# Kernel optimization log

Hardware: AMD Instinct MI355X
Metric: run time of the kernel (lower is better)

Reference implementation:

```python
import jax, jax.numpy as jnp
import numpy as np

H = 25  # fixed state size per module source
N_STEPS = 10


def _lstm_cell(x, h, c, W_ih, W_hh, b_ih, b_hh):
    # PyTorch LSTMCell: gates ordered i, f, g, o
    gates = x @ W_ih.T + b_ih + h @ W_hh.T + b_hh  # [B, 4H]
    i, f, g, o = jnp.split(gates, 4, axis=-1)
    c_new = jax.nn.sigmoid(f) * c + jax.nn.sigmoid(i) * jnp.tanh(g)
    h_new = jax.nn.sigmoid(o) * jnp.tanh(c_new)
    return h_new, c_new


def setup_inputs() -> dict:
    key = jax.random.key(0)
    ks = jax.random.split(key, 11)
    B, A = 131072, 18

    def u(k, shape, fan_in, fan_out):
        bound = np.sqrt(6.0 / (fan_in + fan_out)).astype(np.float32)
        return jax.random.uniform(k, shape, jnp.float32, -bound, bound)

    state = jax.random.normal(ks[0], (B, H), jnp.float32)
    # LSTMCell weights [4H, H]; biases zeroed per module init
    W_ih_enc = u(ks[1], (4 * H, H), H, 4 * H)
    W_hh_enc = u(ks[2], (4 * H, H), H, 4 * H)
    b_ih_enc = jnp.zeros((4 * H,), jnp.float32)
    b_hh_enc = jnp.zeros((4 * H,), jnp.float32)
    W_ih_dec = u(ks[3], (4 * H, H), H, 4 * H)
    W_hh_dec = u(ks[4], (4 * H, H), H, 4 * H)
    b_ih_dec = jnp.zeros((4 * H,), jnp.float32)
    b_hh_dec = jnp.zeros((4 * H,), jnp.float32)
    # actor head: norm_col_init std=0.01, bias 0
    w = jax.random.normal(ks[5], (A, H), jnp.float32)
    W_act = w * (0.01 / jnp.sqrt((w ** 2).sum(1, keepdims=True)))
    b_act = jnp.zeros((A,), jnp.float32)
    return {
        "state_repr_input": state,
        "W_ih_enc": W_ih_enc, "W_hh_enc": W_hh_enc, "b_ih_enc": b_ih_enc, "b_hh_enc": b_hh_enc,
        "W_ih_dec": W_ih_dec, "W_hh_dec": W_hh_dec, "b_ih_dec": b_ih_dec, "b_hh_dec": b_hh_dec,
        "W_act": W_act, "b_act": b_act,
    }


def reference(state_repr_input, W_ih_enc, W_hh_enc, b_ih_enc, b_hh_enc,
              W_ih_dec, W_hh_dec, b_ih_dec, b_hh_dec, W_act, b_act):
    B = state_repr_input.shape[0]
    zeros = jnp.zeros_like(state_repr_input)

    # Encoder: input to each step is previous hx (first step: state)
    def enc_step(carry, _):
        inp, h, c = carry
        h, c = _lstm_cell(inp, h, c, W_ih_enc, W_hh_enc, b_ih_enc, b_hh_enc)
        return (h, h, c), h

    (_, _, _), enc_hs = jax.lax.scan(enc_step, (state_repr_input, zeros, zeros), None, length=N_STEPS)
    # enc_hs: [10, B, 25]

    # Decoder: consumes encoder outputs in order
    def dec_step(carry, x):
        h, c = carry
        h, c = _lstm_cell(x, h, c, W_ih_dec, W_hh_dec, b_ih_dec, b_hh_dec)
        return (h, c), None

    (hx_dec, _), _ = jax.lax.scan(dec_step, (zeros, zeros), enc_hs)

    actor_lang = hx_dec @ W_act.T + b_act  # [B, A]
    return actor_lang, enc_hs
```

## Files before the change

### kernel.cpp

```cpp
#include <hip/hip_runtime.h>


#define HH 25
#define NSTEP 10
#define AOUT 18
#define WPB 4
#define BLK (WPB * 64)
#define NFRG 26
#define LOG2E 1.44269504088896340736f

typedef __attribute__((ext_vector_type(8))) short short8;
typedef __attribute__((ext_vector_type(4))) float f32x4;
typedef __attribute__((ext_vector_type(4))) unsigned u32x4;

__device__ __forceinline__ short f2bf(float x) {
    unsigned u = __float_as_uint(x);
    u += 0x7fffu + ((u >> 16) & 1u);
    return (short)(u >> 16);
}
__device__ __forceinline__ unsigned cvtpk(float lo, float hi) {
    unsigned rr;
    asm("v_cvt_pk_bf16_f32 %0, %1, %2" : "=v"(rr) : "v"(lo), "v"(hi));
    return rr;
}
#if __has_builtin(__builtin_amdgcn_exp2f)
#define EXP2(x) __builtin_amdgcn_exp2f(x)
#else
#define EXP2(x) exp2f(x)
#endif
#define RCP(x) __builtin_amdgcn_rcpf(x)
#define MFMA16(a, b, c) __builtin_amdgcn_mfma_f32_16x16x32_bf16((a), (b), (c), 0, 0, 0)

#define ACT_ELEM(A0, A1, A2, A3, CREF, HOUT)                                   \
    {                                                                          \
        float Ei = EXP2(A0);                                                   \
        float Ef = EXP2(A1);                                                   \
        float Eg = EXP2(A2);                                                   \
        float Eo = EXP2(A3);                                                   \
        float Pf = 1.f + Ef;                                                   \
        float Pig = (1.f + Ei) * (1.f + Eg);                                   \
        float c = fmaf(CREF, Pig, (Eg - 1.f) * Pf) * RCP(Pf * Pig);            \
        CREF = c;                                                              \
        float Ec = EXP2(2.f * LOG2E * c);                                      \
        float Pc = 1.f + Ec;                                                   \
        HOUT = (Pc - 2.f) * RCP(Pc * (1.f + Eo));                              \
    }

__global__ __launch_bounds__(BLK, 4)
void langnn_swap(const float* __restrict__ state,
                 const float* __restrict__ Wih_e, const float* __restrict__ Whh_e,
                 const float* __restrict__ bih_e, const float* __restrict__ bhh_e,
                 const float* __restrict__ Wih_d, const float* __restrict__ Whh_d,
                 const float* __restrict__ bih_d, const float* __restrict__ bhh_d,
                 const float* __restrict__ Wact, const float* __restrict__ bact,
                 float* __restrict__ out, int B)
{
    __shared__ __align__(16) short sFrag[NFRG][64][8];

    const int tid  = threadIdx.x;
    const int lane = tid & 63;
    const int w    = tid >> 6;
    const int r    = lane & 15;
    const int g    = lane >> 4;

    for (int i = tid; i < NFRG * 64; i += BLK) {
        const int idx = i >> 6, l = i & 63;
        const int lj = l & 15, lg = l >> 4;
        const float *W1 = nullptr, *W2 = nullptr, *B1 = nullptr, *B2 = nullptr;
        int gt = 0, hf, rmax = HH;
        if (idx < 8)       { gt = idx >> 1;        hf = idx & 1; W1 = Wih_e; W2 = Whh_e; B1 = bih_e; B2 = bhh_e; }
        else if (idx < 16) { gt = (idx - 8) >> 1;  hf = idx & 1; W1 = Wih_d; B1 = bih_d; B2 = bhh_d; }
        else if (idx < 24) { gt = (idx - 16) >> 1; hf = idx & 1; W1 = Whh_d; }
        else               { hf = idx - 24;        W1 = Wact;    B1 = bact;  rmax = AOUT; }
        const bool actor = (idx >= 24);
        const float sc = actor ? 1.f : (gt == 2 ? 2.f * LOG2E : -LOG2E);
        const int row  = hf * 16 + lj;
        const int nrow = actor ? row : gt * HH + row;
        for (int e = 0; e < 8; ++e) {
            const int k = (e < 4) ? lg * 4 + e : 16 + lg * 4 + (e - 4);
            float v = 0.f;
            if (row < rmax) {
                if (k < HH) {
                    v = W1[nrow * HH + k];
                    if (W2) v += W2[nrow * HH + k];
                    v *= sc;
                } else if (k == 31 && B1) {
                    v = B1[nrow];
                    if (B2) v += B2[nrow];
                    v *= sc;
                }
            }
            sFrag[idx][l][e] = f2bf(v);
        }
    }
    __syncthreads();

    const int b0 = (blockIdx.x * WPB + w) * 16;
    float* encBase = out + (size_t)B * AOUT + (size_t)(b0 + r) * HH;

    float ce[2][4], cd[2][4];
    #pragma unroll
    for (int hf = 0; hf < 2; ++hf)
        #pragma unroll
        for (int q = 0; q < 4; ++q) { ce[hf][q] = 0.f; cd[hf][q] = 0.f; }

    short8 hE, hD;
    {
        const float* sp = state + (size_t)(b0 + r) * HH;
        #pragma unroll
        for (int e = 0; e < 8; ++e) {
            const int k = (e < 4) ? g * 4 + e : 16 + g * 4 + (e - 4);
            hE[e] = (k < HH) ? f2bf(sp[k]) : (k == 31 ? (short)0x3F80 : (short)0);
            hD[e] = (k == 31) ? (short)0x3F80 : (short)0;
        }
    }

    auto actCell = [&](f32x4 (&acc)[8], float (&cc)[2][4], float (&hv)[2][4]) {
        #pragma unroll
        for (int hf = 0; hf < 2; ++hf)
            #pragma unroll
            for (int q = 0; q < 4; ++q)
                ACT_ELEM(acc[0 + hf][q], acc[2 + hf][q], acc[4 + hf][q], acc[6 + hf][q],
                         cc[hf][q], hv[hf][q]);
    };
    auto packH = [&](float (&hv)[2][4]) -> short8 {
        union { u32x4 d; short8 s; } u;
        u.d[0] = cvtpk(hv[0][0], hv[0][1]);
        u.d[1] = cvtpk(hv[0][2], hv[0][3]);
        u.d[2] = cvtpk(hv[1][0], hv[1][1]);
        u.d[3] = cvtpk(hv[1][2], (g == 3) ? 1.0f : hv[1][3]);
        return u.s;
    };
    auto storeEnc = [&](int t, float (&hv)[2][4]) {
        float* p = encBase + (size_t)t * B * HH;
        #pragma unroll
        for (int q = 0; q < 4; ++q) p[g * 4 + q] = hv[0][q];
        #pragma unroll
        for (int q = 0; q < 4; ++q)
            if (g * 4 + q < 9) p[16 + g * 4 + q] = hv[1][q];
    };

    {
        f32x4 acc[8];
        #pragma unroll
        for (int idx = 0; idx < 8; ++idx) {
            const int gt = idx >> 1, hf = idx & 1;
            const float sc = (gt == 2) ? 2.f * LOG2E : -LOG2E;
            const int row = hf * 16 + r;
            short8 Wf;
            #pragma unroll
            for (int e = 0; e < 8; ++e) {
                const int k = (e < 4) ? g * 4 + e : 16 + g * 4 + (e - 4);
                float v = 0.f;
                if (row < HH) {
                    if (k < HH)       v = Wih_e[(gt * HH + row) * HH + k] * sc;
                    else if (k == 31) v = (bih_e[gt * HH + row] + bhh_e[gt * HH + row]) * sc;
                }
                Wf[e] = f2bf(v);
            }
            f32x4 z; z[0] = z[1] = z[2] = z[3] = 0.f;
            acc[idx] = MFMA16(Wf, hE, z);
        }
        float hv[2][4];
        actCell(acc, ce, hv);
        storeEnc(0, hv);
        hE = packH(hv);
    }

    auto decCell = [&]() {
        f32x4 acc[8];
        #pragma unroll
        for (int idx = 0; idx < 8; ++idx) {
            short8 Wx = *(const short8*)&sFrag[8 + idx][lane][0];
            short8 Wh = *(const short8*)&sFrag[16 + idx][lane][0];
            f32x4 z; z[0] = z[1] = z[2] = z[3] = 0.f;
            acc[idx] = MFMA16(Wh, hD, MFMA16(Wx, hE, z));
        }
        float hv[2][4];
        actCell(acc, cd, hv);
        hD = packH(hv);
    };
    auto encCell = [&](int t) {
        f32x4 acc[8];
        #pragma unroll
        for (int idx = 0; idx < 8; ++idx) {
            short8 Wf = *(const short8*)&sFrag[idx][lane][0];
            f32x4 z; z[0] = z[1] = z[2] = z[3] = 0.f;
            acc[idx] = MFMA16(Wf, hE, z);
        }
        float hv[2][4];
        actCell(acc, ce, hv);
        storeEnc(t, hv);
        hE = packH(hv);
    };

    #pragma unroll 1
    for (int t = 0; t < NSTEP - 1; ++t) {
        decCell();
        encCell(t + 1);
    }
    decCell();

    {
        short8 W0 = *(const short8*)&sFrag[24][lane][0];
        short8 W1 = *(const short8*)&sFrag[25][lane][0];
        f32x4 z; z[0] = z[1] = z[2] = z[3] = 0.f;
        f32x4 a0 = MFMA16(W0, hD, z);
        f32x4 a1 = MFMA16(W1, hD, z);
        float* p = out + (size_t)(b0 + r) * AOUT;
        #pragma unroll
        for (int q = 0; q < 4; ++q) p[g * 4 + q] = a0[q];
        #pragma unroll
        for (int q = 0; q < 4; ++q)
            if (16 + g * 4 + q < AOUT) p[16 + g * 4 + q] = a1[q];
    }
}

extern "C" void kernel_launch(void* const* d_in, const int* in_sizes, int n_in,
                              void* d_out, int out_size, void* d_ws, size_t ws_size,
                              hipStream_t stream) {
    const float* state = (const float*)d_in[0];
    const float* Wih_e = (const float*)d_in[1];
    const float* Whh_e = (const float*)d_in[2];
    const float* bih_e = (const float*)d_in[3];
    const float* bhh_e = (const float*)d_in[4];
    const float* Wih_d = (const float*)d_in[5];
    const float* Whh_d = (const float*)d_in[6];
    const float* bih_d = (const float*)d_in[7];
    const float* bhh_d = (const float*)d_in[8];
    const float* Wact  = (const float*)d_in[9];
    const float* bact  = (const float*)d_in[10];

    int B = in_sizes[0] / HH;
    int grid = B / (WPB * 16);

    hipLaunchKernelGGL(langnn_swap, dim3(grid), dim3(BLK), 0, stream,
                       state, Wih_e, Whh_e, bih_e, bhh_e,
                       Wih_d, Whh_d, bih_d, bhh_d, Wact, bact,
                       (float*)d_out, B);
}
```

Measured before the change: 110.1 us.

## Process two 16-row batch tiles per wave to reuse weight fragments and add ILP

Each wave now handles two independent 16-row batch groups, so every weight fragment read from LDS feeds two MFMAs and the two independent recurrences interleave to hide MFMA and transcendental latency. The gate loop is reorganized per half-tile to limit live accumulators, encoder and actor outputs are stored as unaligned 4-wide vector writes, and the grid is halved. Launch bounds drop from 4 to 3 waves per SIMD to leave room for the doubled register state, which lowers occupancy.

```diff
diff --git a/kernel.cpp b/kernel.cpp
--- a/kernel.cpp
+++ b/kernel.cpp
@@ -6,12 +6,14 @@
 #define AOUT 18
 #define WPB 4
 #define BLK (WPB * 64)
+#define NG 2
 #define NFRG 26
 #define LOG2E 1.44269504088896340736f
 
 typedef __attribute__((ext_vector_type(8))) short short8;
 typedef __attribute__((ext_vector_type(4))) float f32x4;
 typedef __attribute__((ext_vector_type(4))) unsigned u32x4;
+typedef float f32x4u __attribute__((ext_vector_type(4), aligned(4)));
 
 __device__ __forceinline__ short f2bf(float x) {
     unsigned u = __float_as_uint(x);
@@ -46,14 +48,14 @@
         HOUT = (Pc - 2.f) * RCP(Pc * (1.f + Eo));                              \
     }
 
-__global__ __launch_bounds__(BLK, 4)
-void langnn_swap(const float* __restrict__ state,
-                 const float* __restrict__ Wih_e, const float* __restrict__ Whh_e,
-                 const float* __restrict__ bih_e, const float* __restrict__ bhh_e,
-                 const float* __restrict__ Wih_d, const float* __restrict__ Whh_d,
-                 const float* __restrict__ bih_d, const float* __restrict__ bhh_d,
-                 const float* __restrict__ Wact, const float* __restrict__ bact,
-                 float* __restrict__ out, int B)
+__global__ __launch_bounds__(BLK, 3)
+void langnn_swap2(const float* __restrict__ state,
+                  const float* __restrict__ Wih_e, const float* __restrict__ Whh_e,
+                  const float* __restrict__ bih_e, const float* __restrict__ bhh_e,
+                  const float* __restrict__ Wih_d, const float* __restrict__ Whh_d,
+                  const float* __restrict__ bih_d, const float* __restrict__ bhh_d,
+                  const float* __restrict__ Wact, const float* __restrict__ bact,
+                  float* __restrict__ out, int B)
 {
     __shared__ __align__(16) short sFrag[NFRG][64][8];
 
@@ -95,103 +97,135 @@
     }
     __syncthreads();
 
-    const int b0 = (blockIdx.x * WPB + w) * 16;
-    float* encBase = out + (size_t)B * AOUT + (size_t)(b0 + r) * HH;
-
-    float ce[2][4], cd[2][4];
+    const int b0 = (blockIdx.x * WPB + w) * (NG * 16);
+
+    float ce[NG][2][4], cd[NG][2][4];
     #pragma unroll
-    for (int hf = 0; hf < 2; ++hf)
-        #pragma unroll
-        for (int q = 0; q < 4; ++q) { ce[hf][q] = 0.f; cd[hf][q] = 0.f; }
-
-    short8 hE, hD;
-    {
-        const float* sp = state + (size_t)(b0 + r) * HH;
+    for (int u = 0; u < NG; ++u)
+        #pragma unroll
+        for (int hf = 0; hf < 2; ++hf)
+            #pragma unroll
+            for (int q = 0; q < 4; ++q) { ce[u][hf][q] = 0.f; cd[u][hf][q] = 0.f; }
+
+    short8 hE[NG], hD[NG];
+    #pragma unroll
+    for (int u = 0; u < NG; ++u) {
+        const float* sp = state + (size_t)(b0 + u * 16 + r) * HH;
         #pragma unroll
         for (int e = 0; e < 8; ++e) {
             const int k = (e < 4) ? g * 4 + e : 16 + g * 4 + (e - 4);
-            hE[e] = (k < HH) ? f2bf(sp[k]) : (k == 31 ? (short)0x3F80 : (short)0);
-            hD[e] = (k == 31) ? (short)0x3F80 : (short)0;
-        }
-    }
-
-    auto actCell = [&](f32x4 (&acc)[8], float (&cc)[2][4], float (&hv)[2][4]) {
-        #pragma unroll
-        for (int hf = 0; hf < 2; ++hf)
-            #pragma unroll
-            for (int q = 0; q < 4; ++q)
-                ACT_ELEM(acc[0 + hf][q], acc[2 + hf][q], acc[4 + hf][q], acc[6 + hf][q],
-                         cc[hf][q], hv[hf][q]);
-    };
+            hE[u][e] = (k < HH) ? f2bf(sp[k]) : (k == 31 ? (short)0x3F80 : (short)0);
+            hD[u][e] = (k == 31) ? (short)0x3F80 : (short)0;
+        }
+    }
+
     auto packH = [&](float (&hv)[2][4]) -> short8 {
-        union { u32x4 d; short8 s; } u;
-        u.d[0] = cvtpk(hv[0][0], hv[0][1]);
-        u.d[1] = cvtpk(hv[0][2], hv[0][3]);
-        u.d[2] = cvtpk(hv[1][0], hv[1][1]);
-        u.d[3] = cvtpk(hv[1][2], (g == 3) ? 1.0f : hv[1][3]);
-        return u.s;
-    };
-    auto storeEnc = [&](int t, float (&hv)[2][4]) {
-        float* p = encBase + (size_t)t * B * HH;
-        #pragma unroll
-        for (int q = 0; q < 4; ++q) p[g * 4 + q] = hv[0][q];
-        #pragma unroll
-        for (int q = 0; q < 4; ++q)
-            if (g * 4 + q < 9) p[16 + g * 4 + q] = hv[1][q];
+        union { u32x4 d; short8 s; } un;
+        un.d[0] = cvtpk(hv[0][0], hv[0][1]);
+        un.d[1] = cvtpk(hv[0][2], hv[0][3]);
+        un.d[2] = cvtpk(hv[1][0], hv[1][1]);
+        un.d[3] = cvtpk(hv[1][2], (g == 3) ? 1.0f : hv[1][3]);
+        return un.s;
+    };
+    auto storeEncHF = [&](int t, int u, int hf, float (&hv4)[4]) {
+        float* p = out + (size_t)B * AOUT + (size_t)t * B * HH + (size_t)(b0 + u * 16 + r) * HH;
+        if (hf == 0) {
+            f32x4u v; v[0] = hv4[0]; v[1] = hv4[1]; v[2] = hv4[2]; v[3] = hv4[3];
+            *(f32x4u*)(p + g * 4) = v;
+        } else {
+            if (g < 2) {
+                f32x4u v; v[0] = hv4[0]; v[1] = hv4[1]; v[2] = hv4[2]; v[3] = hv4[3];
+                *(f32x4u*)(p + 16 + g * 4) = v;
+            } else if (g == 2) {
+                p[24] = hv4[0];
+            }
+        }
     };
 
     {
-        f32x4 acc[8];
-        #pragma unroll
-        for (int idx = 0; idx < 8; ++idx) {
-            const int gt = idx >> 1, hf = idx & 1;
-            const float sc = (gt == 2) ? 2.f * LOG2E : -LOG2E;
-            const int row = hf * 16 + r;
-            short8 Wf;
-            #pragma unroll
-            for (int e = 0; e < 8; ++e) {
-                const int k = (e < 4) ? g * 4 + e : 16 + g * 4 + (e - 4);
-                float v = 0.f;
-                if (row < HH) {
-                    if (k < HH)       v = Wih_e[(gt * HH + row) * HH + k] * sc;
-                    else if (k == 31) v = (bih_e[gt * HH + row] + bhh_e[gt * HH + row]) * sc;
+        float hvE[NG][2][4];
+        #pragma unroll
+        for (int hf = 0; hf < 2; ++hf) {
+            f32x4 acc[NG][4];
+            #pragma unroll
+            for (int gt = 0; gt < 4; ++gt) {
+                const float sc = (gt == 2) ? 2.f * LOG2E : -LOG2E;
+                const int row = hf * 16 + r;
+                short8 Wf;
+                #pragma unroll
+                for (int e = 0; e < 8; ++e) {
+                    const int k = (e < 4) ? g * 4 + e : 16 + g * 4 + (e - 4);
+                    float v = 0.f;
+                    if (row < HH) {
+                        if (k < HH)       v = Wih_e[(gt * HH + row) * HH + k] * sc;
+                        else if (k == 31) v = (bih_e[gt * HH + row] + bhh_e[gt * HH + row]) * sc;
+                    }
+                    Wf[e] = f2bf(v);
                 }
-                Wf[e] = f2bf(v);
-            }
-            f32x4 z; z[0] = z[1] = z[2] = z[3] = 0.f;
-            acc[idx] = MFMA16(Wf, hE, z);
-        }
-        float hv[2][4];
-        actCell(acc, ce, hv);
-        storeEnc(0, hv);
-        hE = packH(hv);
+                f32x4 z; z[0] = z[1] = z[2] = z[3] = 0.f;
+                #pragma unroll
+                for (int u = 0; u < NG; ++u) acc[u][gt] = MFMA16(Wf, hE[u], z);
+            }
+            #pragma unroll
+            for (int u = 0; u < NG; ++u) {
+                #pragma unroll
+                for (int q = 0; q < 4; ++q)
+                    ACT_ELEM(acc[u][0][q], acc[u][1][q], acc[u][2][q], acc[u][3][q],
+                             ce[u][hf][q], hvE[u][hf][q]);
+                storeEncHF(0, u, hf, hvE[u][hf]);
+            }
+        }
+        #pragma unroll
+        for (int u = 0; u < NG; ++u) hE[u] = packH(hvE[u]);
     }
 
     auto decCell = [&]() {
-        f32x4 acc[8];
-        #pragma unroll
-        for (int idx = 0; idx < 8; ++idx) {
-            short8 Wx = *(const short8*)&sFrag[8 + idx][lane][0];
-            short8 Wh = *(const short8*)&sFrag[16 + idx][lane][0];
-            f32x4 z; z[0] = z[1] = z[2] = z[3] = 0.f;
-            acc[idx] = MFMA16(Wh, hD, MFMA16(Wx, hE, z));
-        }
-        float hv[2][4];
-        actCell(acc, cd, hv);
-        hD = packH(hv);
+        float hvD[NG][2][4];
+        #pragma unroll
+        for (int hf = 0; hf < 2; ++hf) {
+            f32x4 acc[NG][4];
+            #pragma unroll
+            for (int gt = 0; gt < 4; ++gt) {
+                short8 Wx = *(const short8*)&sFrag[8 + gt * 2 + hf][lane][0];
+                short8 Wh = *(const short8*)&sFrag[16 + gt * 2 + hf][lane][0];
+                f32x4 z; z[0] = z[1] = z[2] = z[3] = 0.f;
+                #pragma unroll
+                for (int u = 0; u < NG; ++u)
+                    acc[u][gt] = MFMA16(Wh, hD[u], MFMA16(Wx, hE[u], z));
+            }
+            #pragma unroll
+            for (int u = 0; u < NG; ++u)
+                #pragma unroll
+                for (int q = 0; q < 4; ++q)
+                    ACT_ELEM(acc[u][0][q], acc[u][1][q], acc[u][2][q], acc[u][3][q],
+                             cd[u][hf][q], hvD[u][hf][q]);
+        }
+        #pragma unroll
+        for (int u = 0; u < NG; ++u) hD[u] = packH(hvD[u]);
     };
     auto encCell = [&](int t) {
-        f32x4 acc[8];
-        #pragma unroll
-        for (int idx = 0; idx < 8; ++idx) {
-            short8 Wf = *(const short8*)&sFrag[idx][lane][0];
-            f32x4 z; z[0] = z[1] = z[2] = z[3] = 0.f;
-            acc[idx] = MFMA16(Wf, hE, z);
-        }
-        float hv[2][4];
-        actCell(acc, ce, hv);
-        storeEnc(t, hv);
-        hE = packH(hv);
+        float hvE[NG][2][4];
+        #pragma unroll
+        for (int hf = 0; hf < 2; ++hf) {
+            f32x4 acc[NG][4];
+            #pragma unroll
+            for (int gt = 0; gt < 4; ++gt) {
+                short8 Wf = *(const short8*)&sFrag[gt * 2 + hf][lane][0];
+                f32x4 z; z[0] = z[1] = z[2] = z[3] = 0.f;
+                #pragma unroll
+                for (int u = 0; u < NG; ++u) acc[u][gt] = MFMA16(Wf, hE[u], z);
+            }
+            #pragma unroll
+            for (int u = 0; u < NG; ++u) {
+                #pragma unroll
+                for (int q = 0; q < 4; ++q)
+                    ACT_ELEM(acc[u][0][q], acc[u][1][q], acc[u][2][q], acc[u][3][q],
+                             ce[u][hf][q], hvE[u][hf][q]);
+                storeEncHF(t, u, hf, hvE[u][hf]);
+            }
+        }
+        #pragma unroll
+        for (int u = 0; u < NG; ++u) hE[u] = packH(hvE[u]);
     };
 
     #pragma unroll 1
@@ -204,15 +238,16 @@
     {
         short8 W0 = *(const short8*)&sFrag[24][lane][0];
         short8 W1 = *(const short8*)&sFrag[25][lane][0];
-        f32x4 z; z[0] = z[1] = z[2] = z[3] = 0.f;
-        f32x4 a0 = MFMA16(W0, hD, z);
-        f32x4 a1 = MFMA16(W1, hD, z);
-        float* p = out + (size_t)(b0 + r) * AOUT;
-        #pragma unroll
-        for (int q = 0; q < 4; ++q) p[g * 4 + q] = a0[q];
-        #pragma unroll
-        for (int q = 0; q < 4; ++q)
-            if (16 + g * 4 + q < AOUT) p[16 + g * 4 + q] = a1[q];
+        #pragma unroll
+        for (int u = 0; u < NG; ++u) {
+            f32x4 z; z[0] = z[1] = z[2] = z[3] = 0.f;
+            f32x4 a0 = MFMA16(W0, hD[u], z);
+            f32x4 a1 = MFMA16(W1, hD[u], z);
+            float* p = out + (size_t)(b0 + u * 16 + r) * AOUT;
+            f32x4u v; v[0] = a0[0]; v[1] = a0[1]; v[2] = a0[2]; v[3] = a0[3];
+            *(f32x4u*)(p + g * 4) = v;
+            if (g == 0) { p[16] = a1[0]; p[17] = a1[1]; }
+        }
     }
 }
 
@@ -232,9 +267,9 @@
     const float* bact  = (const float*)d_in[10];
 
     int B = in_sizes[0] / HH;
-    int grid = B / (WPB * 16);
-
-    hipLaunchKernelGGL(langnn_swap, dim3(grid), dim3(BLK), 0, stream,
+    int grid = B / (WPB * NG * 16);
+
+    hipLaunchKernelGGL(langnn_swap2, dim3(grid), dim3(BLK), 0, stream,
                        state, Wih_e, Whh_e, bih_e, bhh_e,
                        Wih_d, Whh_d, bih_d, bhh_d, Wact, bact,
                        (float*)d_out, B);
```

New measurement: 101.8 us. -7.5%, faster.

## Hoist LSTM weight fragments to registers and interleave encoder/decoder steps

Applied to the files above, without the earlier changes.

Loads all 24 weight fragments from shared memory into registers once, before the time loop, instead of re-reading them every step. The decoder step t and encoder step t+1 are fused into one loop body so their independent MFMAs and activations can interleave and hide latency. Encoder and actor outputs are written with 4-wide unaligned vector stores instead of scalar stores. Dropping the occupancy hint of 4 in launch bounds lets register use grow, which can lower occupancy.

```diff
diff --git a/kernel.cpp b/kernel.cpp
--- a/kernel.cpp
+++ b/kernel.cpp
@@ -12,6 +12,7 @@
 typedef __attribute__((ext_vector_type(8))) short short8;
 typedef __attribute__((ext_vector_type(4))) float f32x4;
 typedef __attribute__((ext_vector_type(4))) unsigned u32x4;
+typedef float f32x4u __attribute__((ext_vector_type(4), aligned(4)));
 
 __device__ __forceinline__ short f2bf(float x) {
     unsigned u = __float_as_uint(x);
@@ -46,14 +47,14 @@
         HOUT = (Pc - 2.f) * RCP(Pc * (1.f + Eo));                              \
     }
 
-__global__ __launch_bounds__(BLK, 4)
-void langnn_swap(const float* __restrict__ state,
-                 const float* __restrict__ Wih_e, const float* __restrict__ Whh_e,
-                 const float* __restrict__ bih_e, const float* __restrict__ bhh_e,
-                 const float* __restrict__ Wih_d, const float* __restrict__ Whh_d,
-                 const float* __restrict__ bih_d, const float* __restrict__ bhh_d,
-                 const float* __restrict__ Wact, const float* __restrict__ bact,
-                 float* __restrict__ out, int B)
+__global__ __launch_bounds__(BLK)
+void langnn_reg(const float* __restrict__ state,
+                const float* __restrict__ Wih_e, const float* __restrict__ Whh_e,
+                const float* __restrict__ bih_e, const float* __restrict__ bhh_e,
+                const float* __restrict__ Wih_d, const float* __restrict__ Whh_d,
+                const float* __restrict__ bih_d, const float* __restrict__ bhh_d,
+                const float* __restrict__ Wact, const float* __restrict__ bact,
+                float* __restrict__ out, int B)
 {
     __shared__ __align__(16) short sFrag[NFRG][64][8];
 
@@ -95,8 +96,15 @@
     }
     __syncthreads();
 
+    short8 We[8], Wx[8], Wh[8];
+    #pragma unroll
+    for (int i = 0; i < 8; ++i) {
+        We[i] = *(const short8*)&sFrag[i][lane][0];
+        Wx[i] = *(const short8*)&sFrag[8 + i][lane][0];
+        Wh[i] = *(const short8*)&sFrag[16 + i][lane][0];
+    }
+
     const int b0 = (blockIdx.x * WPB + w) * 16;
-    float* encBase = out + (size_t)B * AOUT + (size_t)(b0 + r) * HH;
 
     float ce[2][4], cd[2][4];
     #pragma unroll
@@ -115,91 +123,103 @@
         }
     }
 
-    auto actCell = [&](f32x4 (&acc)[8], float (&cc)[2][4], float (&hv)[2][4]) {
-        #pragma unroll
-        for (int hf = 0; hf < 2; ++hf)
-            #pragma unroll
-            for (int q = 0; q < 4; ++q)
-                ACT_ELEM(acc[0 + hf][q], acc[2 + hf][q], acc[4 + hf][q], acc[6 + hf][q],
-                         cc[hf][q], hv[hf][q]);
-    };
     auto packH = [&](float (&hv)[2][4]) -> short8 {
-        union { u32x4 d; short8 s; } u;
-        u.d[0] = cvtpk(hv[0][0], hv[0][1]);
-        u.d[1] = cvtpk(hv[0][2], hv[0][3]);
-        u.d[2] = cvtpk(hv[1][0], hv[1][1]);
-        u.d[3] = cvtpk(hv[1][2], (g == 3) ? 1.0f : hv[1][3]);
-        return u.s;
+        union { u32x4 d; short8 s; } un;
+        un.d[0] = cvtpk(hv[0][0], hv[0][1]);
+        un.d[1] = cvtpk(hv[0][2], hv[0][3]);
+        un.d[2] = cvtpk(hv[1][0], hv[1][1]);
+        un.d[3] = cvtpk(hv[1][2], (g == 3) ? 1.0f : hv[1][3]);
+        return un.s;
     };
     auto storeEnc = [&](int t, float (&hv)[2][4]) {
-        float* p = encBase + (size_t)t * B * HH;
-        #pragma unroll
-        for (int q = 0; q < 4; ++q) p[g * 4 + q] = hv[0][q];
-        #pragma unroll
-        for (int q = 0; q < 4; ++q)
-            if (g * 4 + q < 9) p[16 + g * 4 + q] = hv[1][q];
+        float* p = out + (size_t)B * AOUT + (size_t)t * B * HH + (size_t)(b0 + r) * HH;
+        { f32x4u v; v[0] = hv[0][0]; v[1] = hv[0][1]; v[2] = hv[0][2]; v[3] = hv[0][3];
+          *(f32x4u*)(p + g * 4) = v; }
+        if (g < 2) {
+            f32x4u v; v[0] = hv[1][0]; v[1] = hv[1][1]; v[2] = hv[1][2]; v[3] = hv[1][3];
+            *(f32x4u*)(p + 16 + g * 4) = v;
+        } else if (g == 2) {
+            p[24] = hv[1][0];
+        }
     };
 
     {
-        f32x4 acc[8];
-        #pragma unroll
-        for (int idx = 0; idx < 8; ++idx) {
-            const int gt = idx >> 1, hf = idx & 1;
-            const float sc = (gt == 2) ? 2.f * LOG2E : -LOG2E;
-            const int row = hf * 16 + r;
-            short8 Wf;
-            #pragma unroll
-            for (int e = 0; e < 8; ++e) {
-                const int k = (e < 4) ? g * 4 + e : 16 + g * 4 + (e - 4);
-                float v = 0.f;
-                if (row < HH) {
-                    if (k < HH)       v = Wih_e[(gt * HH + row) * HH + k] * sc;
-                    else if (k == 31) v = (bih_e[gt * HH + row] + bhh_e[gt * HH + row]) * sc;
+        f32x4 acc[2][4];
+        #pragma unroll
+        for (int hf = 0; hf < 2; ++hf)
+            #pragma unroll
+            for (int gt = 0; gt < 4; ++gt) {
+                const float sc = (gt == 2) ? 2.f * LOG2E : -LOG2E;
+                const int row = hf * 16 + r;
+                short8 Wf;
+                #pragma unroll
+                for (int e = 0; e < 8; ++e) {
+                    const int k = (e < 4) ? g * 4 + e : 16 + g * 4 + (e - 4);
+                    float v = 0.f;
+                    if (row < HH) {
+                        if (k < HH)       v = Wih_e[(gt * HH + row) * HH + k] * sc;
+                        else if (k == 31) v = (bih_e[gt * HH + row] + bhh_e[gt * HH + row]) * sc;
+                    }
+                    Wf[e] = f2bf(v);
                 }
-                Wf[e] = f2bf(v);
-            }
-            f32x4 z; z[0] = z[1] = z[2] = z[3] = 0.f;
-            acc[idx] = MFMA16(Wf, hE, z);
-        }
+                f32x4 z; z[0] = z[1] = z[2] = z[3] = 0.f;
+                acc[hf][gt] = MFMA16(Wf, hE, z);
+            }
         float hv[2][4];
-        actCell(acc, ce, hv);
+        #pragma unroll
+        for (int hf = 0; hf < 2; ++hf)
+            #pragma unroll
+            for (int q = 0; q < 4; ++q)
+                ACT_ELEM(acc[hf][0][q], acc[hf][1][q], acc[hf][2][q], acc[hf][3][q],
+                         ce[hf][q], hv[hf][q]);
         storeEnc(0, hv);
         hE = packH(hv);
     }
 
-    auto decCell = [&]() {
-        f32x4 acc[8];
-        #pragma unroll
-        for (int idx = 0; idx < 8; ++idx) {
-            short8 Wx = *(const short8*)&sFrag[8 + idx][lane][0];
-            short8 Wh = *(const short8*)&sFrag[16 + idx][lane][0];
-            f32x4 z; z[0] = z[1] = z[2] = z[3] = 0.f;
-            acc[idx] = MFMA16(Wh, hD, MFMA16(Wx, hE, z));
-        }
-        float hv[2][4];
-        actCell(acc, cd, hv);
-        hD = packH(hv);
-    };
-    auto encCell = [&](int t) {
-        f32x4 acc[8];
-        #pragma unroll
-        for (int idx = 0; idx < 8; ++idx) {
-            short8 Wf = *(const short8*)&sFrag[idx][lane][0];
-            f32x4 z; z[0] = z[1] = z[2] = z[3] = 0.f;
-            acc[idx] = MFMA16(Wf, hE, z);
-        }
-        float hv[2][4];
-        actCell(acc, ce, hv);
-        storeEnc(t, hv);
-        hE = packH(hv);
-    };
-
     #pragma unroll 1
     for (int t = 0; t < NSTEP - 1; ++t) {
-        decCell();
-        encCell(t + 1);
-    }
-    decCell();
+        f32x4 accD[2][4], accE[2][4];
+        #pragma unroll
+        for (int hf = 0; hf < 2; ++hf)
+            #pragma unroll
+            for (int gt = 0; gt < 4; ++gt) {
+                f32x4 z; z[0] = z[1] = z[2] = z[3] = 0.f;
+                accD[hf][gt] = MFMA16(Wh[gt * 2 + hf], hD, MFMA16(Wx[gt * 2 + hf], hE, z));
+                accE[hf][gt] = MFMA16(We[gt * 2 + hf], hE, z);
+            }
+        float hvD[2][4], hvE[2][4];
+        #pragma unroll
+        for (int hf = 0; hf < 2; ++hf)
+            #pragma unroll
+            for (int q = 0; q < 4; ++q) {
+                ACT_ELEM(accD[hf][0][q], accD[hf][1][q], accD[hf][2][q], accD[hf][3][q],
+                         cd[hf][q], hvD[hf][q]);
+                ACT_ELEM(accE[hf][0][q], accE[hf][1][q], accE[hf][2][q], accE[hf][3][q],
+                         ce[hf][q], hvE[hf][q]);
+            }
+        storeEnc(t + 1, hvE);
+        hD = packH(hvD);
+        hE = packH(hvE);
+    }
+
+    {
+        f32x4 acc[2][4];
+        #pragma unroll
+        for (int hf = 0; hf < 2; ++hf)
+            #pragma unroll
+            for (int gt = 0; gt < 4; ++gt) {
+                f32x4 z; z[0] = z[1] = z[2] = z[3] = 0.f;
+                acc[hf][gt] = MFMA16(Wh[gt * 2 + hf], hD, MFMA16(Wx[gt * 2 + hf], hE, z));
+            }
+        float hv[2][4];
+        #pragma unroll
+        for (int hf = 0; hf < 2; ++hf)
+            #pragma unroll
+            for (int q = 0; q < 4; ++q)
+                ACT_ELEM(acc[hf][0][q], acc[hf][1][q], acc[hf][2][q], acc[hf][3][q],
+                         cd[hf][q], hv[hf][q]);
+        hD = packH(hv);
+    }
 
     {
         short8 W0 = *(const short8*)&sFrag[24][lane][0];
@@ -208,11 +228,9 @@
         f32x4 a0 = MFMA16(W0, hD, z);
         f32x4 a1 = MFMA16(W1, hD, z);
         float* p = out + (size_t)(b0 + r) * AOUT;
-        #pragma unroll
-        for (int q = 0; q < 4; ++q) p[g * 4 + q] = a0[q];
-        #pragma unroll
-        for (int q = 0; q < 4; ++q)
-            if (16 + g * 4 + q < AOUT) p[16 + g * 4 + q] = a1[q];
+        f32x4u v; v[0] = a0[0]; v[1] = a0[1]; v[2] = a0[2]; v[3] = a0[3];
+        *(f32x4u*)(p + g * 4) = v;
+        if (g == 0) { p[16] = a1[0]; p[17] = a1[1]; }
     }
 }
 
@@ -234,7 +252,7 @@
     int B = in_sizes[0] / HH;
     int grid = B / (WPB * 16);
 
-    hipLaunchKernelGGL(langnn_swap, dim3(grid), dim3(BLK), 0, stream,
+    hipLaunchKernelGGL(langnn_reg, dim3(grid), dim3(BLK), 0, stream,
                        state, Wih_e, Whh_e, bih_e, bhh_e,
                        Wih_d, Whh_d, bih_d, bhh_d, Wact, bact,
                        (float*)d_out, B);
```

Result: slower. 130.2 us (+18.3%).
